# Kernel tuning notes

Hardware: AMD Instinct MI355X
Metric: run time of the kernel (lower is better)

## Reference

```python
import jax, jax.numpy as jnp
import numpy as np

INPUT_DIM = 128
BATCH = 4096
N_FORMULAS = 256
N_CONJ_ARR = [6, 9, 12, 15]
DEPTH_ARR = [2, 4, 6]
KEEP_PROB_ARR = [0.1, 0.3, 0.5, 0.7, 0.9]
EPS = 1.0  # binary_threshold_eps


def _build_structure():
    # Formulas split evenly across the 4 conjunction-count groups; each formula's
    # conjunctions split evenly across the 3 depths. Each literal belongs to exactly
    # one conjunction; each conjunction to exactly one formula (block-sparse structure).
    group = N_FORMULAS // len(N_CONJ_ARR)
    f_of_l, c_of_l, f_of_c = [], [], []
    cid = 0
    for f in range(N_FORMULAS):
        nc = N_CONJ_ARR[f // group]
        for d in DEPTH_ARR:
            for _ in range(nc // len(DEPTH_ARR)):
                f_of_c.append(f)
                f_of_l.extend([f] * d)
                c_of_l.extend([cid] * d)
                cid += 1
    return (np.array(f_of_l, np.int32), np.array(c_of_l, np.int32),
            np.array(f_of_c, np.int32))


def setup_inputs() -> dict:
    f_of_l, c_of_l, f_of_c = _build_structure()
    L = f_of_l.shape[0]  # 10752 literals
    rng = np.random.default_rng(0)
    # generate_random_mask: per-formula keep prob cycles through KEEP_PROB_ARR,
    # feature mask is Bernoulli(p) per formula, extended to every literal of that formula.
    p = np.array([KEEP_PROB_ARR[f % len(KEEP_PROB_ARR)] for f in range(N_FORMULAS)])
    formulas_random_mask = (rng.random((INPUT_DIM, N_FORMULAS)) < p).astype(np.float32)
    literals_random_mask = formulas_random_mask[:, f_of_l]  # (D, L)
    fan = INPUT_DIM + L
    glorot = rng.normal(0.0, np.sqrt(2.0 / fan), size=(INPUT_DIM, L)).astype(np.float32)
    key = jax.random.key(0)
    kx, kmu, ksig = jax.random.split(key, 3)
    return {
        "x": jax.random.normal(kx, (BATCH, INPUT_DIM), dtype=jnp.float32),
        # build(): self.weight = glorot_weight * literals_random_mask
        "weight": jnp.asarray(glorot * literals_random_mask),
        "bias": jnp.zeros((L,), jnp.float32),
        # learnable_mask initialized to binary_threshold_eps + 0.5
        "learnable_mask": jnp.full((INPUT_DIM, N_FORMULAS), EPS + 0.5, jnp.float32),
        # keras random_normal initializer default stddev = 0.05
        "mu": 0.05 * jax.random.normal(kmu, (N_FORMULAS, INPUT_DIM), dtype=jnp.float32),
        "sigma": 0.05 * jax.random.normal(ksig, (1, N_FORMULAS, INPUT_DIM), dtype=jnp.float32),
        "temperature": jnp.full((1,), 2.0, jnp.float32),
        "formula_of_literal": jnp.asarray(f_of_l),
        "conj_of_literal": jnp.asarray(c_of_l),
        "formula_of_conj": jnp.asarray(f_of_c),
    }


def reference(x, weight, bias, learnable_mask, mu, sigma, temperature,
              formula_of_literal, conj_of_literal, formula_of_conj):
    L = weight.shape[1]
    n_conj = formula_of_conj.shape[0]
    n_formulas = mu.shape[0]
    dt = weight.dtype

    # FeatureSelection: binary threshold + extension-matrix sparse matmul (gather form)
    mask01 = (jnp.abs(learnable_mask) > EPS).astype(dt)          # (D, F)
    learnable_binary_mask = mask01[:, formula_of_literal]        # (D, L) == M01 @ ext_matrix

    # and/or biases = column sums of the 0/1 indicator matrices
    and_bias = jax.ops.segment_sum(jnp.ones((L,), dt), conj_of_literal, num_segments=n_conj)
    or_bias = jax.ops.segment_sum(jnp.ones((n_conj,), dt), formula_of_conj, num_segments=n_formulas)

    # literals: tanh(x @ (W * M) + b)
    out_literals = jnp.tanh(x @ (weight * learnable_binary_mask) + bias)  # (B, L)

    # sparse indicator matmuls as segment sums over the literal/conjunction axis
    conj_sum = jax.ops.segment_sum(out_literals.T, conj_of_literal, num_segments=n_conj).T  # (B, C)
    out_conjunctions = jnp.tanh(conj_sum - and_bias + 1.5)       # soft AND
    form_sum = jax.ops.segment_sum(out_conjunctions.T, formula_of_conj, num_segments=n_formulas).T
    out_dnnfs = jnp.tanh(form_sum + or_bias - 1.5)               # soft OR, (B, F)

    # Localization: RBF distance -> sigmoid(temperature)-scaled softmax
    diff = x[:, None, :] - mu[None, :, :]                        # (B, F, D)
    loc = jnp.exp(-jnp.linalg.norm(diff * sigma, axis=-1))       # (B, F)
    loc = jax.nn.softmax(jax.nn.sigmoid(temperature) * loc, axis=-1)

    return out_dnnfs * loc
```

## Files before the change

kernel.cpp:

```cpp
#include <hip/hip_runtime.h>

#define L_TOT 10752
#define NF    256
#define BATCHN 4096

typedef __attribute__((ext_vector_type(8))) short short8;
typedef __attribute__((ext_vector_type(4))) float f32x4;

__device__ __forceinline__ unsigned short f2bf(float f) {
  unsigned int u = __float_as_uint(f);
  unsigned int r = (u + 0x7FFFu + ((u >> 16) & 1u)) >> 16;
  return (unsigned short)r;
}

__device__ __forceinline__ float tanh_fast(float x) {
  float e2 = __builtin_amdgcn_exp2f(x * 2.8853900817779268f);
  float r  = __builtin_amdgcn_rcpf(e2 + 1.0f);
  return fmaf(-2.0f, r, 1.0f);
}

template<int G> struct Sch;
template<> struct Sch<0> {
  static constexpr int NT = 2, NC = 6;
  static constexpr int p6[2]  = {0b11, 0};
  static constexpr int m4[2]  = {0, 0b0011};
  static constexpr int m2a[2] = {0, 0b0100};
  static constexpr int m2b[2] = {0, 0b0100};
};
template<> struct Sch<1> {
  static constexpr int NT = 3, NC = 9;
  static constexpr int p6[3]  = {0b11, 0b01, 0};
  static constexpr int m4[3]  = {0, 0b1100, 0b0001};
  static constexpr int m2a[3] = {0, 0, 0b0110};
  static constexpr int m2b[3] = {0, 0, 0b0010};
};
template<> struct Sch<2> {
  static constexpr int NT = 4, NC = 12;
  static constexpr int p6[4]  = {0b11, 0b11, 0, 0};
  static constexpr int m4[4]  = {0, 0, 0b1111, 0};
  static constexpr int m2a[4] = {0, 0, 0, 0b0011};
  static constexpr int m2b[4] = {0, 0, 0, 0b0011};
};
template<> struct Sch<3> {
  static constexpr int NT = 5, NC = 15;
  static constexpr int p6[5]  = {0b11, 0b11, 0b01, 0, 0};
  static constexpr int m4[5]  = {0, 0, 0b1100, 0b0111, 0};
  static constexpr int m2a[5] = {0, 0, 0, 0b1000, 0b0011};
  static constexpr int m2b[5] = {0, 0, 0, 0b1000, 0b0001};
};

template<int G>
__device__ __forceinline__ void prep_w_body(
    const float* __restrict__ weight, const float* __restrict__ bias,
    const float* __restrict__ lm, int f, int ls, int fbase, int k0,
    unsigned short* __restrict__ WT, float* __restrict__ bias_p,
    unsigned short* s_t)
{
  using S = Sch<G>;
  constexpr int n3 = S::NC / 3;
  constexpr int LF = 12 * n3;
  constexpr int NROWS = S::NT * 16;
  const int tid = threadIdx.x;
  for (int e = tid; e < 64 * LF; e += 512) {
    int kk = e / LF;
    int j = e - kk * LF;
    int k = k0 + kk;
    float m = (fabsf(lm[k * NF + f]) > 1.0f) ? 1.0f : 0.0f;
    s_t[j * 72 + kk] = f2bf(weight[(size_t)k * L_TOT + ls + j] * m);
  }
  __syncthreads();
  const int kk = tid & 63, rb = tid >> 6;
  for (int R = rb; R < NROWS; R += 8) {
    int j = -1;
    if (R < 8 * n3)        { int dd = R & 7; if (dd < 6) j = 6 * n3 + 6 * (R >> 3) + dd; }
    else if (R < 12 * n3)  j = R - 6 * n3;
    else if (R < 14 * n3)  j = R - 12 * n3;
    unsigned short v = (j >= 0) ? s_t[j * 72 + kk] : (unsigned short)0;
    WT[(size_t)(fbase + R) * 128 + k0 + kk] = v;
    if (kk == 0 && k0 == 0) bias_p[fbase + R] = (j >= 0) ? bias[ls + j] : 0.0f;
  }
}

__global__ __launch_bounds__(512) void prep_all(
    const float4* __restrict__ x4, ushort4* __restrict__ a2,
    const float* __restrict__ mu, const float* __restrict__ sigma,
    unsigned short* __restrict__ B2, float* __restrict__ cf,
    const float* __restrict__ weight, const float* __restrict__ bias,
    const float* __restrict__ lm,
    unsigned short* __restrict__ WT, float* __restrict__ bias_p)
{
  __shared__ unsigned short s_t[60 * 72];
  int bi = blockIdx.x, tid = threadIdx.x;
  if (bi < 256) {
    int i = bi * 512 + tid;
    float4 v = x4[i];
    int b = i >> 5, kc = i & 31;
    ushort4 sq, xx;
    sq.x = f2bf(v.x * v.x); sq.y = f2bf(v.y * v.y);
    sq.z = f2bf(v.z * v.z); sq.w = f2bf(v.w * v.w);
    xx.x = f2bf(v.x); xx.y = f2bf(v.y); xx.z = f2bf(v.z); xx.w = f2bf(v.w);
    a2[b * 64 + kc] = sq;
    a2[b * 64 + 32 + kc] = xx;
  } else if (bi < 288) {
    int f = (bi - 256) * 8 + (tid >> 6);
    int k = tid & 63;
    float acc = 0.0f;
    for (int kk = k; kk < 128; kk += 64) {
      float s = sigma[f * 128 + kk], m = mu[f * 128 + kk];
      float s2 = s * s;
      B2[f * 256 + kk] = f2bf(s2);
      B2[f * 256 + 128 + kk] = f2bf(-2.0f * m * s2);
      acc = fmaf(m * m, s2, acc);
    }
    for (int o = 1; o < 64; o <<= 1) acc += __shfl_xor(acc, o);
    if (k == 0) cf[f] = acc;
  } else {
    int idx = bi - 288;
    int f = idx >> 1, k0 = (idx & 1) * 64;
    int g = f >> 6, fo = f & 63;
    if (g == 0)      prep_w_body<0>(weight, bias, lm, f, 0    + fo * 24, fo * 32,        k0, WT, bias_p, s_t);
    else if (g == 1) prep_w_body<1>(weight, bias, lm, f, 1536 + fo * 36, 2048 + fo * 48, k0, WT, bias_p, s_t);
    else if (g == 2) prep_w_body<2>(weight, bias, lm, f, 3840 + fo * 48, 5120 + fo * 64, k0, WT, bias_p, s_t);
    else             prep_w_body<3>(weight, bias, lm, f, 6912 + fo * 60, 9216 + fo * 80, k0, WT, bias_p, s_t);
  }
}

__device__ __forceinline__ short8 ldsw(const unsigned short* s_w, int row, int colb) {
  int off = (row << 8) + (colb ^ ((row & 7) << 4));
  return *reinterpret_cast<const short8*>(reinterpret_cast<const char*>(s_w) + off);
}

template<int G>
__device__ __forceinline__ void mfma_stage(const unsigned short* s_w, const float* s_bias,
                                           const short8* xc, f32x4& acc, int t, int n, int q)
{
  acc = *reinterpret_cast<const f32x4*>(&s_bias[t * 16 + q * 4]);
#pragma unroll
  for (int kk = 0; kk < 4; ++kk)
    acc = __builtin_amdgcn_mfma_f32_16x16x32_bf16(
        ldsw(s_w, t * 16 + n, kk * 64 + q * 16), xc[kk], acc, 0, 0, 0);
}

template<int G>
__device__ __forceinline__ void reduce_stage(const f32x4& ac, float& fs, int t, int q)
{
  using S = Sch<G>;
  float v0 = tanh_fast(ac[0]);
  float v1 = tanh_fast(ac[1]);
  float v2 = tanh_fast(ac[2]);
  float v3 = tanh_fast(ac[3]);
  float s = v0 + v1 + v2 + v3;
  if (S::p6[t]) {
    float po = __shfl_xor(s, 16);
    float t6 = tanh_fast(s + po - 4.5f);
    bool add = ((q & 1) == 0) && ((S::p6[t] >> (q >> 1)) & 1);
    fs += add ? t6 : 0.0f;
  }
  if (S::m4[t]) {
    float t4 = tanh_fast(s - 2.5f);
    fs += ((S::m4[t] >> q) & 1) ? t4 : 0.0f;
  }
  if (S::m2a[t]) {
    float ta = tanh_fast(v0 + v1 - 0.5f);
    fs += ((S::m2a[t] >> q) & 1) ? ta : 0.0f;
  }
  if (S::m2b[t]) {
    float tb = tanh_fast(v2 + v3 - 0.5f);
    fs += ((S::m2b[t] >> q) & 1) ? tb : 0.0f;
  }
}

template<int G>
__device__ __forceinline__ void dnnf_body(
    const unsigned short* __restrict__ A2,
    const unsigned short* __restrict__ WT,
    const float* __restrict__ bias_p,
    float* __restrict__ dnnf,
    int f, int fbase, int batch0,
    unsigned short* s_w, float* s_bias)
{
  using S = Sch<G>;
  constexpr int NT = S::NT;
  constexpr int NS = 8 * NT;
  const int tid = threadIdx.x;
  const int lane = tid & 63;
  const int wv = tid >> 6;
  const int n = lane & 15;
  const int q = lane >> 4;

  const char* wsrc = reinterpret_cast<const char*>(WT + (size_t)fbase * 128);
#pragma unroll
  for (int p = 0; p < NT; ++p) {
    int c = p * 256 + tid;
    int row = c >> 4;
    int lin = c << 4;
    int swz = lin ^ ((row & 7) << 4);
    uint4 v = *reinterpret_cast<const uint4*>(wsrc + lin);
    *reinterpret_cast<uint4*>(reinterpret_cast<char*>(s_w) + swz) = v;
  }
  if (tid < NT * 16) s_bias[tid] = bias_p[fbase + tid];
  __syncthreads();

  const unsigned short* xr0 = A2 + (size_t)(batch0 + wv * 16 + n) * 256 + 128;
  short8 x0[4], x1[4];
  f32x4 a0, a1;
  float fs = 0.0f;

#pragma unroll
  for (int kk = 0; kk < 4; ++kk)
    x0[kk] = *reinterpret_cast<const short8*>(xr0 + kk * 32 + q * 8);
  mfma_stage<G>(s_w, s_bias, x0, a0, 0, n, q);

#pragma unroll
  for (int s = 0; s < NS; ++s) {
    const int it = s / NT, t = s - it * NT;
    if (t == NT - 2 && it < 7) {
      const unsigned short* xr = xr0 + (size_t)(it + 1) * 64 * 256;
      if (((it + 1) & 1) == 0) {
#pragma unroll
        for (int kk = 0; kk < 4; ++kk)
          x0[kk] = *reinterpret_cast<const short8*>(xr + kk * 32 + q * 8);
      } else {
#pragma unroll
        for (int kk = 0; kk < 4; ++kk)
          x1[kk] = *reinterpret_cast<const short8*>(xr + kk * 32 + q * 8);
      }
    }
    if (s + 1 < NS) {
      const int it1 = (s + 1) / NT;
      const int t1 = (s + 1) - it1 * NT;
      if (((s + 1) & 1) == 0) {
        if ((it1 & 1) == 0) mfma_stage<G>(s_w, s_bias, x0, a0, t1, n, q);
        else                mfma_stage<G>(s_w, s_bias, x1, a0, t1, n, q);
      } else {
        if ((it1 & 1) == 0) mfma_stage<G>(s_w, s_bias, x0, a1, t1, n, q);
        else                mfma_stage<G>(s_w, s_bias, x1, a1, t1, n, q);
      }
    }
    if ((s & 1) == 0) reduce_stage<G>(a0, fs, t, q);
    else              reduce_stage<G>(a1, fs, t, q);
    if (t == NT - 1) {
      fs += __shfl_xor(fs, 16);
      fs += __shfl_xor(fs, 32);
      float dv = tanh_fast(fs + (float)S::NC - 1.5f);
      if (lane < 16)
        dnnf[(size_t)f * BATCHN + batch0 + it * 64 + wv * 16 + n] = dv;
      fs = 0.0f;
    }
  }
}

__global__ __launch_bounds__(256, 2) void dnnf_main(
    const unsigned short* __restrict__ A2,
    const unsigned short* __restrict__ WT,
    const float* __restrict__ bias_p,
    float* __restrict__ dnnf)
{
  __shared__ __align__(16) unsigned short s_w[80 * 128];
  __shared__ __align__(16) float s_bias[80];
  int bi = blockIdx.x;
  int u = bi >> 3;
  int batch0 = (bi & 7) * 512;
  int g = u & 3, fo = u >> 2;
  int f = (g << 6) | fo;
  if (g == 0)      dnnf_body<0>(A2, WT, bias_p, dnnf, f, fo * 32,        batch0, s_w, s_bias);
  else if (g == 1) dnnf_body<1>(A2, WT, bias_p, dnnf, f, 2048 + fo * 48, batch0, s_w, s_bias);
  else if (g == 2) dnnf_body<2>(A2, WT, bias_p, dnnf, f, 5120 + fo * 64, batch0, s_w, s_bias);
  else             dnnf_body<3>(A2, WT, bias_p, dnnf, f, 9216 + fo * 80, batch0, s_w, s_bias);
}

__global__ __launch_bounds__(1024) void loc_fused(
    const unsigned short* __restrict__ A2,
    const unsigned short* __restrict__ B2,
    const float* __restrict__ cf,
    const float* __restrict__ temp,
    const float* __restrict__ dnnf,
    float* __restrict__ out)
{
  __shared__ float s_part[16][16];
  __shared__ float s_d[256 * 17];
  int tid = threadIdx.x, lane = tid & 63, w = tid >> 6, n = lane & 15, q = lane >> 4;
  int b0 = blockIdx.x * 16;

  {
    int fr = tid >> 2, c4 = (tid & 3) * 4;
    f32x4 v = *reinterpret_cast<const f32x4*>(dnnf + (size_t)fr * BATCHN + b0 + c4);
    s_d[fr * 17 + c4 + 0] = v[0];
    s_d[fr * 17 + c4 + 1] = v[1];
    s_d[fr * 17 + c4 + 2] = v[2];
    s_d[fr * 17 + c4 + 3] = v[3];
  }

  const unsigned short* arow = A2 + (size_t)(b0 + n) * 256;
  const unsigned short* brow = B2 + (size_t)(w * 16 + n) * 256;
  f32x4 acc = (f32x4){0.f, 0.f, 0.f, 0.f};
#pragma unroll
  for (int kk = 0; kk < 8; ++kk) {
    short8 af = *reinterpret_cast<const short8*>(arow + kk * 32 + q * 8);
    short8 bf = *reinterpret_cast<const short8*>(brow + kk * 32 + q * 8);
    acc = __builtin_amdgcn_mfma_f32_16x16x32_bf16(af, bf, acc, 0, 0, 0);
  }

  float T = temp[0];
  float sg = 1.0f / (1.0f + __builtin_amdgcn_exp2f(-T * 1.4426950408889634f));
  float ez[4];
  float sr[4];
  float c = cf[w * 16 + n];
#pragma unroll
  for (int r = 0; r < 4; ++r) {
    float n2 = fmaxf(acc[r] + c, 0.0f);
    float loc = __builtin_amdgcn_exp2f(-__builtin_amdgcn_sqrtf(n2) * 1.4426950408889634f);
    float e = __builtin_amdgcn_exp2f(sg * loc * 1.4426950408889634f);
    ez[r] = e;
    sr[r] = e;
  }
#pragma unroll
  for (int o = 1; o < 16; o <<= 1)
#pragma unroll
    for (int r = 0; r < 4; ++r) sr[r] += __shfl_xor(sr[r], o);
  if (n == 0) {
#pragma unroll
    for (int r = 0; r < 4; ++r) s_part[w][q * 4 + r] = sr[r];
  }
  __syncthreads();
  float rtot[4];
#pragma unroll
  for (int r = 0; r < 4; ++r) {
    float tot = 0.0f;
#pragma unroll
    for (int ww = 0; ww < 16; ++ww) tot += s_part[ww][q * 4 + r];
    rtot[r] = 1.0f / tot;
  }
  int fc = w * 16 + n;
#pragma unroll
  for (int r = 0; r < 4; ++r) {
    int bg = b0 + q * 4 + r;
    out[(size_t)bg * 256 + fc] = s_d[fc * 17 + q * 4 + r] * ez[r] * rtot[r];
  }
}

extern "C" void kernel_launch(void* const* d_in, const int* in_sizes, int n_in,
                              void* d_out, int out_size, void* d_ws, size_t ws_size,
                              hipStream_t stream) {
  const float* x      = (const float*)d_in[0];
  const float* weight = (const float*)d_in[1];
  const float* bias   = (const float*)d_in[2];
  const float* lm     = (const float*)d_in[3];
  const float* mu     = (const float*)d_in[4];
  const float* sigma  = (const float*)d_in[5];
  const float* temp   = (const float*)d_in[6];
  float* out = (float*)d_out;

  char* ws = (char*)d_ws;
  unsigned short* A2     = (unsigned short*)(ws);
  float*          dnnf   = (float*)(ws + 2097152);
  unsigned short* B2     = (unsigned short*)(ws + 6291456);
  float*          cf     = (float*)(ws + 6422528);
  unsigned short* WT     = (unsigned short*)(ws + 6423552);
  float*          bias_p = (float*)(ws + 10093568);

  prep_all<<<800, 512, 0, stream>>>((const float4*)x, (ushort4*)A2,
                                    mu, sigma, B2, cf,
                                    weight, bias, lm, WT, bias_p);
  dnnf_main<<<2048, 256, 0, stream>>>(A2, WT, bias_p, dnnf);
  loc_fused<<<256, 1024, 0, stream>>>(A2, B2, cf, temp, dnnf, out);
}
```

Before: 133.0 us.

## Replace software-pipelined MFMA loop with simple rolled loop for higher occupancy

Removes the hand-pipelined double-buffered MFMA/reduce schedule and replaces it with a non-unrolled per-batch-chunk loop. Each chunk loads the x fragments, runs the MFMAs under raised wave priority, and applies the bias after accumulation. Launch bounds go from 2 to 4 blocks per CU so the hardware can hide latency through more resident waves instead of through explicit software prefetch. The risk is exposed global-load latency per iteration if the extra occupancy does not materialise or is not enough to cover it.

```diff
diff --git a/kernel.cpp b/kernel.cpp
--- a/kernel.cpp
+++ b/kernel.cpp
@@ -131,46 +131,6 @@
 }
 
 template<int G>
-__device__ __forceinline__ void mfma_stage(const unsigned short* s_w, const float* s_bias,
-                                           const short8* xc, f32x4& acc, int t, int n, int q)
-{
-  acc = *reinterpret_cast<const f32x4*>(&s_bias[t * 16 + q * 4]);
-#pragma unroll
-  for (int kk = 0; kk < 4; ++kk)
-    acc = __builtin_amdgcn_mfma_f32_16x16x32_bf16(
-        ldsw(s_w, t * 16 + n, kk * 64 + q * 16), xc[kk], acc, 0, 0, 0);
-}
-
-template<int G>
-__device__ __forceinline__ void reduce_stage(const f32x4& ac, float& fs, int t, int q)
-{
-  using S = Sch<G>;
-  float v0 = tanh_fast(ac[0]);
-  float v1 = tanh_fast(ac[1]);
-  float v2 = tanh_fast(ac[2]);
-  float v3 = tanh_fast(ac[3]);
-  float s = v0 + v1 + v2 + v3;
-  if (S::p6[t]) {
-    float po = __shfl_xor(s, 16);
-    float t6 = tanh_fast(s + po - 4.5f);
-    bool add = ((q & 1) == 0) && ((S::p6[t] >> (q >> 1)) & 1);
-    fs += add ? t6 : 0.0f;
-  }
-  if (S::m4[t]) {
-    float t4 = tanh_fast(s - 2.5f);
-    fs += ((S::m4[t] >> q) & 1) ? t4 : 0.0f;
-  }
-  if (S::m2a[t]) {
-    float ta = tanh_fast(v0 + v1 - 0.5f);
-    fs += ((S::m2a[t] >> q) & 1) ? ta : 0.0f;
-  }
-  if (S::m2b[t]) {
-    float tb = tanh_fast(v2 + v3 - 0.5f);
-    fs += ((S::m2b[t] >> q) & 1) ? tb : 0.0f;
-  }
-}
-
-template<int G>
 __device__ __forceinline__ void dnnf_body(
     const unsigned short* __restrict__ A2,
     const unsigned short* __restrict__ WT,
@@ -181,7 +141,6 @@
 {
   using S = Sch<G>;
   constexpr int NT = S::NT;
-  constexpr int NS = 8 * NT;
   const int tid = threadIdx.x;
   const int lane = tid & 63;
   const int wv = tid >> 6;
@@ -201,56 +160,61 @@
   if (tid < NT * 16) s_bias[tid] = bias_p[fbase + tid];
   __syncthreads();
 
-  const unsigned short* xr0 = A2 + (size_t)(batch0 + wv * 16 + n) * 256 + 128;
-  short8 x0[4], x1[4];
-  f32x4 a0, a1;
-  float fs = 0.0f;
-
-#pragma unroll
-  for (int kk = 0; kk < 4; ++kk)
-    x0[kk] = *reinterpret_cast<const short8*>(xr0 + kk * 32 + q * 8);
-  mfma_stage<G>(s_w, s_bias, x0, a0, 0, n, q);
-
-#pragma unroll
-  for (int s = 0; s < NS; ++s) {
-    const int it = s / NT, t = s - it * NT;
-    if (t == NT - 2 && it < 7) {
-      const unsigned short* xr = xr0 + (size_t)(it + 1) * 64 * 256;
-      if (((it + 1) & 1) == 0) {
-#pragma unroll
-        for (int kk = 0; kk < 4; ++kk)
-          x0[kk] = *reinterpret_cast<const short8*>(xr + kk * 32 + q * 8);
-      } else {
-#pragma unroll
-        for (int kk = 0; kk < 4; ++kk)
-          x1[kk] = *reinterpret_cast<const short8*>(xr + kk * 32 + q * 8);
+  const unsigned short* xr = A2 + (size_t)(batch0 + wv * 16 + n) * 256 + 128;
+  float* dst = dnnf + (size_t)f * BATCHN + batch0 + wv * 16 + n;
+  const float* bp = s_bias + q * 4;
+
+#pragma unroll 1
+  for (int it = 0; it < 8; ++it) {
+    short8 xc[4];
+#pragma unroll
+    for (int kk = 0; kk < 4; ++kk)
+      xc[kk] = *reinterpret_cast<const short8*>(xr + kk * 32 + q * 8);
+
+    float fs = 0.0f;
+#pragma unroll
+    for (int t = 0; t < NT; ++t) {
+      f32x4 acc = (f32x4){0.f, 0.f, 0.f, 0.f};
+      __builtin_amdgcn_s_setprio(1);
+#pragma unroll
+      for (int kk = 0; kk < 4; ++kk)
+        acc = __builtin_amdgcn_mfma_f32_16x16x32_bf16(
+            ldsw(s_w, t * 16 + n, kk * 64 + q * 16), xc[kk], acc, 0, 0, 0);
+      __builtin_amdgcn_s_setprio(0);
+      float v0 = tanh_fast(acc[0] + bp[t * 16 + 0]);
+      float v1 = tanh_fast(acc[1] + bp[t * 16 + 1]);
+      float v2 = tanh_fast(acc[2] + bp[t * 16 + 2]);
+      float v3 = tanh_fast(acc[3] + bp[t * 16 + 3]);
+      float s = v0 + v1 + v2 + v3;
+      if (S::p6[t]) {
+        float po = __shfl_xor(s, 16);
+        float t6 = tanh_fast(s + po - 4.5f);
+        bool add = ((q & 1) == 0) && ((S::p6[t] >> (q >> 1)) & 1);
+        fs += add ? t6 : 0.0f;
+      }
+      if (S::m4[t]) {
+        float t4 = tanh_fast(s - 2.5f);
+        fs += ((S::m4[t] >> q) & 1) ? t4 : 0.0f;
+      }
+      if (S::m2a[t]) {
+        float ta = tanh_fast(v0 + v1 - 0.5f);
+        fs += ((S::m2a[t] >> q) & 1) ? ta : 0.0f;
+      }
+      if (S::m2b[t]) {
+        float tb = tanh_fast(v2 + v3 - 0.5f);
+        fs += ((S::m2b[t] >> q) & 1) ? tb : 0.0f;
       }
     }
-    if (s + 1 < NS) {
-      const int it1 = (s + 1) / NT;
-      const int t1 = (s + 1) - it1 * NT;
-      if (((s + 1) & 1) == 0) {
-        if ((it1 & 1) == 0) mfma_stage<G>(s_w, s_bias, x0, a0, t1, n, q);
-        else                mfma_stage<G>(s_w, s_bias, x1, a0, t1, n, q);
-      } else {
-        if ((it1 & 1) == 0) mfma_stage<G>(s_w, s_bias, x0, a1, t1, n, q);
-        else                mfma_stage<G>(s_w, s_bias, x1, a1, t1, n, q);
-      }
-    }
-    if ((s & 1) == 0) reduce_stage<G>(a0, fs, t, q);
-    else              reduce_stage<G>(a1, fs, t, q);
-    if (t == NT - 1) {
-      fs += __shfl_xor(fs, 16);
-      fs += __shfl_xor(fs, 32);
-      float dv = tanh_fast(fs + (float)S::NC - 1.5f);
-      if (lane < 16)
-        dnnf[(size_t)f * BATCHN + batch0 + it * 64 + wv * 16 + n] = dv;
-      fs = 0.0f;
-    }
-  }
-}
-
-__global__ __launch_bounds__(256, 2) void dnnf_main(
+    fs += __shfl_xor(fs, 16);
+    fs += __shfl_xor(fs, 32);
+    float dv = tanh_fast(fs + (float)S::NC - 1.5f);
+    if (lane < 16) *dst = dv;
+    xr += 64 * 256;
+    dst += 64;
+  }
+}
+
+__global__ __launch_bounds__(256, 4) void dnnf_main(
     const unsigned short* __restrict__ A2,
     const unsigned short* __restrict__ WT,
     const float* __restrict__ bias_p,
```

Measured after the change: 137.2 us. 1.03x slower.

## Move localization softmax into main kernel blocks and apply dnnf in a final multiply pass

Applied to the files above, without the earlier changes.

Adds 256 extra blocks to the dnnf kernel. They compute the RBF localization softmax with 256-thread blocks, four 16-column MFMA tiles per wave, and write the softmax result directly to the output. The last kernel now only reads dnnf and multiplies it into the output in place. The goal is to overlap the localization work with the dnnf computation instead of running it serially after it. The cost is an extra read-modify-write pass over the output, and the new blocks may compete with the dnnf blocks for occupancy.

```diff
diff --git a/kernel.cpp b/kernel.cpp
--- a/kernel.cpp
+++ b/kernel.cpp
@@ -250,15 +250,91 @@
   }
 }
 
-__global__ __launch_bounds__(256, 2) void dnnf_main(
+__device__ __forceinline__ void locsm_body(
+    const unsigned short* __restrict__ A2,
+    const unsigned short* __restrict__ B2,
+    const float* __restrict__ cf,
+    const float* __restrict__ temp,
+    float* __restrict__ out,
+    int b0, float (*s_part)[16])
+{
+  int tid = threadIdx.x, lane = tid & 63, w = tid >> 6, n = lane & 15, q = lane >> 4;
+  const unsigned short* arow = A2 + (size_t)(b0 + n) * 256;
+  f32x4 acc[4];
+#pragma unroll
+  for (int t = 0; t < 4; ++t) acc[t] = (f32x4){0.f, 0.f, 0.f, 0.f};
+#pragma unroll
+  for (int kk = 0; kk < 8; ++kk) {
+    short8 af = *reinterpret_cast<const short8*>(arow + kk * 32 + q * 8);
+#pragma unroll
+    for (int t = 0; t < 4; ++t) {
+      const unsigned short* brow = B2 + (size_t)(w * 64 + t * 16 + n) * 256;
+      short8 bf = *reinterpret_cast<const short8*>(brow + kk * 32 + q * 8);
+      acc[t] = __builtin_amdgcn_mfma_f32_16x16x32_bf16(af, bf, acc[t], 0, 0, 0);
+    }
+  }
+  float T = temp[0];
+  float sg = 1.0f / (1.0f + __builtin_amdgcn_exp2f(-T * 1.4426950408889634f));
+  float ez[4][4];
+  float sr[4] = {0.f, 0.f, 0.f, 0.f};
+#pragma unroll
+  for (int t = 0; t < 4; ++t) {
+    float c = cf[w * 64 + t * 16 + n];
+#pragma unroll
+    for (int r = 0; r < 4; ++r) {
+      float n2 = fmaxf(acc[t][r] + c, 0.0f);
+      float loc = __builtin_amdgcn_exp2f(-__builtin_amdgcn_sqrtf(n2) * 1.4426950408889634f);
+      float e = __builtin_amdgcn_exp2f(sg * loc * 1.4426950408889634f);
+      ez[t][r] = e;
+      sr[r] += e;
+    }
+  }
+#pragma unroll
+  for (int o = 1; o < 16; o <<= 1)
+#pragma unroll
+    for (int r = 0; r < 4; ++r) sr[r] += __shfl_xor(sr[r], o);
+  if (n == 0) {
+#pragma unroll
+    for (int r = 0; r < 4; ++r) s_part[w][q * 4 + r] = sr[r];
+  }
+  __syncthreads();
+  float rtot[4];
+#pragma unroll
+  for (int r = 0; r < 4; ++r) {
+    float tot = s_part[0][q * 4 + r] + s_part[1][q * 4 + r] +
+                s_part[2][q * 4 + r] + s_part[3][q * 4 + r];
+    rtot[r] = 1.0f / tot;
+  }
+#pragma unroll
+  for (int t = 0; t < 4; ++t) {
+    int fc = w * 64 + t * 16 + n;
+#pragma unroll
+    for (int r = 0; r < 4; ++r) {
+      int bg = b0 + q * 4 + r;
+      out[(size_t)bg * 256 + fc] = ez[t][r] * rtot[r];
+    }
+  }
+}
+
+__global__ __launch_bounds__(256, 2) void main2(
     const unsigned short* __restrict__ A2,
     const unsigned short* __restrict__ WT,
     const float* __restrict__ bias_p,
-    float* __restrict__ dnnf)
+    const unsigned short* __restrict__ B2,
+    const float* __restrict__ cf,
+    const float* __restrict__ temp,
+    float* __restrict__ dnnf,
+    float* __restrict__ out)
 {
   __shared__ __align__(16) unsigned short s_w[80 * 128];
   __shared__ __align__(16) float s_bias[80];
+  __shared__ float s_part[4][16];
   int bi = blockIdx.x;
+  if (bi < 256) {
+    locsm_body(A2, B2, cf, temp, out, bi * 16, s_part);
+    return;
+  }
+  bi -= 256;
   int u = bi >> 3;
   int batch0 = (bi & 7) * 512;
   int g = u & 3, fo = u >> 2;
@@ -269,19 +345,11 @@
   else             dnnf_body<3>(A2, WT, bias_p, dnnf, f, 9216 + fo * 80, batch0, s_w, s_bias);
 }
 
-__global__ __launch_bounds__(1024) void loc_fused(
-    const unsigned short* __restrict__ A2,
-    const unsigned short* __restrict__ B2,
-    const float* __restrict__ cf,
-    const float* __restrict__ temp,
-    const float* __restrict__ dnnf,
-    float* __restrict__ out)
-{
-  __shared__ float s_part[16][16];
+__global__ __launch_bounds__(1024) void mult(
+    const float* __restrict__ dnnf, float* __restrict__ out)
+{
   __shared__ float s_d[256 * 17];
-  int tid = threadIdx.x, lane = tid & 63, w = tid >> 6, n = lane & 15, q = lane >> 4;
-  int b0 = blockIdx.x * 16;
-
+  int tid = threadIdx.x, b0 = blockIdx.x * 16;
   {
     int fr = tid >> 2, c4 = (tid & 3) * 4;
     f32x4 v = *reinterpret_cast<const f32x4*>(dnnf + (size_t)fr * BATCHN + b0 + c4);
@@ -290,52 +358,12 @@
     s_d[fr * 17 + c4 + 2] = v[2];
     s_d[fr * 17 + c4 + 3] = v[3];
   }
-
-  const unsigned short* arow = A2 + (size_t)(b0 + n) * 256;
-  const unsigned short* brow = B2 + (size_t)(w * 16 + n) * 256;
-  f32x4 acc = (f32x4){0.f, 0.f, 0.f, 0.f};
-#pragma unroll
-  for (int kk = 0; kk < 8; ++kk) {
-    short8 af = *reinterpret_cast<const short8*>(arow + kk * 32 + q * 8);
-    short8 bf = *reinterpret_cast<const short8*>(brow + kk * 32 + q * 8);
-    acc = __builtin_amdgcn_mfma_f32_16x16x32_bf16(af, bf, acc, 0, 0, 0);
-  }
-
-  float T = temp[0];
-  float sg = 1.0f / (1.0f + __builtin_amdgcn_exp2f(-T * 1.4426950408889634f));
-  float ez[4];
-  float sr[4];
-  float c = cf[w * 16 + n];
-#pragma unroll
-  for (int r = 0; r < 4; ++r) {
-    float n2 = fmaxf(acc[r] + c, 0.0f);
-    float loc = __builtin_amdgcn_exp2f(-__builtin_amdgcn_sqrtf(n2) * 1.4426950408889634f);
-    float e = __builtin_amdgcn_exp2f(sg * loc * 1.4426950408889634f);
-    ez[r] = e;
-    sr[r] = e;
-  }
-#pragma unroll
-  for (int o = 1; o < 16; o <<= 1)
-#pragma unroll
-    for (int r = 0; r < 4; ++r) sr[r] += __shfl_xor(sr[r], o);
-  if (n == 0) {
-#pragma unroll
-    for (int r = 0; r < 4; ++r) s_part[w][q * 4 + r] = sr[r];
-  }
   __syncthreads();
-  float rtot[4];
-#pragma unroll
-  for (int r = 0; r < 4; ++r) {
-    float tot = 0.0f;
-#pragma unroll
-    for (int ww = 0; ww < 16; ++ww) tot += s_part[ww][q * 4 + r];
-    rtot[r] = 1.0f / tot;
-  }
-  int fc = w * 16 + n;
-#pragma unroll
-  for (int r = 0; r < 4; ++r) {
-    int bg = b0 + q * 4 + r;
-    out[(size_t)bg * 256 + fc] = s_d[fc * 17 + q * 4 + r] * ez[r] * rtot[r];
+  int f = tid & 255, bb = tid >> 8;
+#pragma unroll
+  for (int i = 0; i < 4; ++i) {
+    int b = bb * 4 + i;
+    out[(size_t)(b0 + b) * 256 + f] *= s_d[f * 17 + b];
   }
 }
 
@@ -362,6 +390,6 @@
   prep_all<<<800, 512, 0, stream>>>((const float4*)x, (ushort4*)A2,
                                     mu, sigma, B2, cf,
                                     weight, bias, lm, WT, bias_p);
-  dnnf_main<<<2048, 256, 0, stream>>>(A2, WT, bias_p, dnnf);
-  loc_fused<<<256, 1024, 0, stream>>>(A2, B2, cf, temp, dnnf, out);
-}
+  main2<<<2304, 256, 0, stream>>>(A2, WT, bias_p, B2, cf, temp, dnnf, out);
+  mult<<<256, 1024, 0, stream>>>(dnnf, out);
+}
```

After: 130.5 us. About the same (-1.8%).
